# Optimization experiments

Measured on AMD Instinct MI355X. Metric: run time of the kernel, lower is better.

## Reference

```python
import jax, jax.numpy as jnp
import numpy as np

NUM_Q_HEADS = 64
NUM_KV_HEADS = 8
HEAD_DIM = 64
HIDDEN = 2880
SLIDING_WINDOW = 128
ROPE_WAVELENGTH = 10000.0
NEG_INF = jnp.float32(-1e9)


def _rope(x, start_index=0):
    # x: (b, s, n, h). yarn with scaling_factor=1.0 == standard RoPE (split-half rotate).
    s, h = x.shape[1], x.shape[-1]
    inv_freq = 1.0 / (ROPE_WAVELENGTH ** (jnp.arange(0, h, 2, dtype=jnp.float32) / h))
    pos = jnp.arange(s, dtype=jnp.float32) + start_index
    freqs = pos[:, None] * inv_freq[None, :]  # (s, h/2)
    cos = jnp.concatenate([jnp.cos(freqs), jnp.cos(freqs)], axis=-1)[None, :, None, :]
    sin = jnp.concatenate([jnp.sin(freqs), jnp.sin(freqs)], axis=-1)[None, :, None, :]
    x1, x2 = jnp.split(x, 2, axis=-1)
    rot = jnp.concatenate([-x2, x1], axis=-1)
    return x * cos + rot * sin


def setup_inputs() -> dict:
    key = jax.random.key(0)
    ks = jax.random.split(key, 9)
    b, s = 1, 2048
    scale = 0.02
    hidden_states = jax.random.normal(ks[0], (b, s, HIDDEN), jnp.float32)
    Wq = jax.random.normal(ks[1], (HIDDEN, NUM_Q_HEADS, HEAD_DIM), jnp.float32) * scale
    Wk = jax.random.normal(ks[2], (HIDDEN, NUM_KV_HEADS, HEAD_DIM), jnp.float32) * scale
    Wv = jax.random.normal(ks[3], (HIDDEN, NUM_KV_HEADS, HEAD_DIM), jnp.float32) * scale
    Wo = jax.random.normal(ks[4], (NUM_Q_HEADS, HEAD_DIM, HIDDEN), jnp.float32) * scale
    bq = jnp.zeros((NUM_Q_HEADS, HEAD_DIM), jnp.float32)
    bk = jnp.zeros((NUM_KV_HEADS, HEAD_DIM), jnp.float32)
    bv = jnp.zeros((NUM_KV_HEADS, HEAD_DIM), jnp.float32)
    bo = jnp.zeros((HIDDEN,), jnp.float32)
    sinks = jax.random.normal(ks[5], (NUM_Q_HEADS,), jnp.float32) * 0.05
    attention_mask = jnp.tril(jnp.ones((s, s), bool))[None]  # causal, (b, q, k)
    return dict(hidden_states=hidden_states, Wq=Wq, bq=bq, Wk=Wk, bk=bk, Wv=Wv,
                bv=bv, Wo=Wo, bo=bo, sinks=sinks, attention_mask=attention_mask)


def reference(hidden_states, Wq, bq, Wk, bk, Wv, bv, Wo, bo, sinks, attention_mask):
    b, s, _ = hidden_states.shape
    inv_norm = 1.0 / np.sqrt(HEAD_DIM).astype(np.float32)
    # QKV projections (EinsumDense with bias)
    q = jnp.einsum('bqm,muh->bquh', hidden_states, Wq) + bq
    k = jnp.einsum('bkm,mvh->bkvh', hidden_states, Wk) + bk
    v = jnp.einsum('bkm,mvh->bkvh', hidden_states, Wv) + bv
    # rotary_dim == head_dim (even), so RoPE applies to the full head dim
    q = _rope(q)
    k = _rope(k)
    # GQA: repeat kv heads
    groups = NUM_Q_HEADS // NUM_KV_HEADS
    k = jnp.repeat(k, groups, axis=2)
    v = jnp.repeat(v, groups, axis=2)
    scores = jnp.einsum('bquh,bkuh->buqk', q, k) * inv_norm
    # sliding-window mask: keep kv_pos >= q_pos - window
    qpos = jnp.arange(s)
    swin = qpos[None, :] >= qpos[:, None] - SLIDING_WINDOW  # (q, k)
    scores = jnp.where(swin[None, None], scores, NEG_INF)
    scores = jnp.where(attention_mask[:, None], scores, NEG_INF)
    # sink-token logit per head appended as extra kv column
    sink = jnp.broadcast_to(sinks.reshape(1, NUM_Q_HEADS, 1, 1), (b, NUM_Q_HEADS, s, 1))
    logits = jnp.concatenate([scores, sink], axis=-1)
    m = jax.lax.stop_gradient(jnp.max(logits, axis=-1, keepdims=True))
    probs = jax.nn.softmax(logits - m, axis=-1)[..., :-1]  # drop sink column
    attn = jnp.einsum('buqk,bkuh->bquh', probs, v)
    return jnp.einsum('bquh,uhm->bqm', attn, Wo) + bo
```

## Files before the change

kernel.cpp:

```cpp
#include <hip/hip_runtime.h>
#include <cstdint>

typedef __attribute__((ext_vector_type(4))) float f32x4;
typedef __attribute__((ext_vector_type(8))) short bf16x8;

#define HIDDEN 2880
#define SEQ 2048
#define QKV_N 5120
#define WIN 128

__device__ __forceinline__ ushort f2bf(float f) {
  uint32_t u = __builtin_bit_cast(uint32_t, f);
  u += 0x7fff + ((u >> 16) & 1);
  return (ushort)(u >> 16);
}
__device__ __forceinline__ float bf2f(ushort h) {
  uint32_t u = ((uint32_t)h) << 16;
  return __builtin_bit_cast(float, u);
}

__global__ void conv_kernel(const float* __restrict__ in, ushort* __restrict__ out, int n) {
  int i = (blockIdx.x * blockDim.x + threadIdx.x) * 8;
  if (i >= n) return;
  float4 a = *(const float4*)(in + i);
  float4 b = *(const float4*)(in + i + 4);
  bf16x8 o;
  o[0] = (short)f2bf(a.x); o[1] = (short)f2bf(a.y); o[2] = (short)f2bf(a.z); o[3] = (short)f2bf(a.w);
  o[4] = (short)f2bf(b.x); o[5] = (short)f2bf(b.y); o[6] = (short)f2bf(b.z); o[7] = (short)f2bf(b.w);
  *(bf16x8*)(out + i) = o;
}

__global__ __launch_bounds__(256) void tconv2_kernel(const float* __restrict__ in, ushort* __restrict__ out,
                                                     int C, int out_ld, int out_row_off) {
  __shared__ ushort tile[64][68];
  int c0 = blockIdx.x * 64, r0 = blockIdx.y * 64;
  int t = threadIdx.x;
  int lr = t >> 4;
  int lc = (t & 15) * 4;
#pragma unroll
  for (int i = 0; i < 4; ++i) {
    float4 v = *(const float4*)&in[(size_t)(r0 + i * 16 + lr) * C + c0 + lc];
    ushort4 o;
    o.x = f2bf(v.x); o.y = f2bf(v.y); o.z = f2bf(v.z); o.w = f2bf(v.w);
    *(ushort4*)&tile[i * 16 + lr][lc] = o;
  }
  __syncthreads();
  int rr0 = (t & 7) * 8;
#pragma unroll
  for (int i2 = 0; i2 < 2; ++i2) {
    int cc = i2 * 32 + (t >> 3);
    bf16x8 o;
#pragma unroll
    for (int j = 0; j < 8; ++j) o[j] = (short)tile[rr0 + j][cc];
    *(bf16x8*)&out[(size_t)(out_row_off + c0 + cc) * out_ld + r0 + rr0] = o;
  }
}

__global__ void biascat_kernel(const float* __restrict__ bq, const float* __restrict__ bk,
                               const float* __restrict__ bv, float* __restrict__ out) {
  int i = blockIdx.x * blockDim.x + threadIdx.x;
  if (i >= QKV_N) return;
  float v = (i < 4096) ? bq[i] : (i < 4608) ? bk[i - 4096] : bv[i - 4608];
  out[i] = v;
}

__global__ void ropetab_kernel(float2* __restrict__ tab) {
  int i = blockIdx.x * blockDim.x + threadIdx.x;
  int s = i >> 5, d = i & 31;
  float inv = powf(10000.0f, -(float)d / 32.0f);
  float f = (float)s * inv;
  tab[i] = make_float2(cosf(f), sinf(f));
}

__global__ void rope8_kernel(ushort* __restrict__ buf, const float2* __restrict__ tab,
                             int perrow , int total) {
  int idx = blockIdx.x * blockDim.x + threadIdx.x;
  if (idx >= total) return;
  int s = idx / perrow;
  int p = idx - s * perrow;
  int head = p >> 2, j = p & 3;
  ushort* base = buf + (size_t)s * QKV_N + head * 64 + j * 8;
  bf16x8 x1 = *(const bf16x8*)base;
  bf16x8 x2 = *(const bf16x8*)(base + 32);
  bf16x8 o1, o2;
#pragma unroll
  for (int i = 0; i < 8; ++i) {
    float2 cs = tab[(s << 5) + j * 8 + i];
    float a = bf2f((ushort)x1[i]), b = bf2f((ushort)x2[i]);
    o1[i] = (short)f2bf(a * cs.x - b * cs.y);
    o2[i] = (short)f2bf(b * cs.x + a * cs.y);
  }
  *(bf16x8*)base = o1;
  *(bf16x8*)(base + 32) = o2;
}

__global__ __launch_bounds__(256) void vt_kernel(const ushort* __restrict__ qkv, ushort* __restrict__ vt) {
  __shared__ ushort tile[64][80];
  int kv0 = blockIdx.x * 64, d0 = blockIdx.y * 64;
  int t = threadIdx.x;
#pragma unroll
  for (int p = 0; p < 2; ++p) {
    int lr = p * 32 + (t >> 3);
    *(bf16x8*)&tile[lr][(t & 7) * 8] =
        *(const bf16x8*)&qkv[(size_t)(kv0 + lr) * QKV_N + 4608 + d0 + (t & 7) * 8];
  }
  __syncthreads();
#pragma unroll
  for (int p = 0; p < 2; ++p) {
    int dl = p * 32 + (t >> 3);
    bf16x8 o;
#pragma unroll
    for (int jj = 0; jj < 8; ++jj) o[jj] = (short)tile[(t & 7) * 8 + jj][dl];
    *(bf16x8*)&vt[(size_t)(d0 + dl) * 2048 + kv0 + (t & 7) * 8] = o;
  }
}

template <int BN, bool OUT_BF16>
__global__ __launch_bounds__(256, 2) void gemm4w_kernel(
    const ushort* __restrict__ A, const ushort* __restrict__ Bt,
    const float* __restrict__ bias, void* __restrict__ Cv,
    int K, int lda, int ldb, int ldc) {
  constexpr int NFRAG = BN / 32;
  constexpr int BHALF = BN * 64;
  constexpr int BCHUNKS = BHALF / 1024;
  constexpr int BUFBYTES = 16384 + 2 * BHALF;
  __shared__ __align__(16) char ldsbuf[2 * BUFBYTES];

  const int cpx = gridDim.x >> 3;
  const int wg = ((int)blockIdx.x & 7) * cpx + ((int)blockIdx.x >> 3);
  const int mtile = wg & 15, ntile = wg >> 4;
  const int m0 = mtile * 128, n0 = ntile * BN;

  const int tid = threadIdx.x, wv = tid >> 6, l = tid & 63;
  const int wm = wv >> 1, wn = wv & 1;
  const int r = l & 15, g = l >> 4;

  const int c = l ^ ((l >> 3) & 3);
  const ushort* gA0 = A + (size_t)(m0 + (c >> 2)) * lda + (c & 3) * 8;
  const ushort* gB0 = Bt + (size_t)(n0 + (c >> 2)) * ldb + (c & 3) * 8;

  const int gsw = (g * 16) ^ (((r >> 1) & 3) << 4);
  const int aOff = (wm * 64 + r) * 64 + gsw;
  const int bOff = (wn * (NFRAG * 16) + r) * 64 + gsw;

  auto sA = [&](int nb, int kg, int kh) {
#pragma unroll
    for (int j = 0; j < 2; ++j) {
      int cid = j * 4 + wv;
      __builtin_amdgcn_global_load_lds(
          (const __attribute__((address_space(1))) void*)(const void*)(gA0 + (size_t)cid * 16 * lda + kg),
          (__attribute__((address_space(3))) void*)&ldsbuf[nb * BUFBYTES + kh * 8192 + cid * 1024], 16, 0, 0);
    }
  };
  auto sB = [&](int nb, int kg, int kh) {
#pragma unroll
    for (int j = 0; j < (BCHUNKS + 3) / 4; ++j) {
      int cid = j * 4 + wv;
      if (cid < BCHUNKS)
        __builtin_amdgcn_global_load_lds(
            (const __attribute__((address_space(1))) void*)(const void*)(gB0 + (size_t)cid * 16 * ldb + kg),
            (__attribute__((address_space(3))) void*)&ldsbuf[nb * BUFBYTES + 16384 + kh * BHALF + cid * 1024],
            16, 0, 0);
    }
  };

#define BAR() __builtin_amdgcn_s_barrier()
#define LGKM0()                                              \
  do {                                                       \
    asm volatile("s_waitcnt lgkmcnt(0)" ::: "memory");       \
    __builtin_amdgcn_sched_barrier(0);                       \
  } while (0)
#define WAITV0() asm volatile("s_waitcnt vmcnt(0)" ::: "memory")

  f32x4 acc[4][NFRAG] = {};
  const int nt = K >> 6;

  sA(0, 0, 0); sA(0, 32, 1); sB(0, 0, 0); sB(0, 32, 1);
  WAITV0();
  BAR();

  for (int t = 0; t < nt; ++t) {
    const int bufOff = (t & 1) * BUFBYTES;
    const int nb = (t & 1) ^ 1;
    if (t + 1 < nt) {
      const int kn = (t + 1) * 64;
      sA(nb, kn, 0); sA(nb, kn + 32, 1);
      sB(nb, kn, 0); sB(nb, kn + 32, 1);
    }
#pragma unroll
    for (int kh = 0; kh < 2; ++kh) {
      bf16x8 aq[4], bq[NFRAG];
#pragma unroll
      for (int nf = 0; nf < NFRAG; ++nf)
        bq[nf] = *(const bf16x8*)&ldsbuf[bufOff + 16384 + kh * BHALF + bOff + nf * 1024];
#pragma unroll
      for (int mi = 0; mi < 4; ++mi)
        aq[mi] = *(const bf16x8*)&ldsbuf[bufOff + kh * 8192 + aOff + mi * 1024];
      LGKM0();
      __builtin_amdgcn_s_setprio(1);
#pragma unroll
      for (int mi = 0; mi < 4; ++mi)
#pragma unroll
        for (int nf = 0; nf < NFRAG; ++nf)
          acc[mi][nf] = __builtin_amdgcn_mfma_f32_16x16x32_bf16(aq[mi], bq[nf], acc[mi][nf], 0, 0, 0);
      __builtin_amdgcn_s_setprio(0);
    }
    WAITV0();
    BAR();
  }

#pragma unroll
  for (int mf2 = 0; mf2 < 4; ++mf2) {
#pragma unroll
    for (int nf = 0; nf < NFRAG; ++nf) {
      int cc = n0 + wn * (NFRAG * 16) + nf * 16 + r;
      float b = bias[cc];
#pragma unroll
      for (int j = 0; j < 4; ++j) {
        int rrow = m0 + wm * 64 + mf2 * 16 + g * 4 + j;
        float v = acc[mf2][nf][j] + b;
        if (OUT_BF16) ((ushort*)Cv)[(size_t)rrow * ldc + cc] = f2bf(v);
        else ((float*)Cv)[(size_t)rrow * ldc + cc] = v;
      }
    }
  }
#undef BAR
#undef LGKM0
#undef WAITV0
}

__global__ __launch_bounds__(512, 4) void attn_kernel(
    const ushort* __restrict__ qkv, const ushort* __restrict__ vt,
    const float* __restrict__ sinks, ushort* __restrict__ out) {
  __shared__ __align__(16) char lds[54272];
  const int kh = blockIdx.y;
  const int q0 = blockIdx.x * 32;
  const int kvw0 = q0 - 128;
  const int tid = threadIdx.x, w = tid >> 6, l = tid & 63;
  const int r = l & 15, g = l >> 4;
  const int h = kh * 8 + w;

  if (tid < 256) ((uint32_t*)(lds + 40960))[tid] = 0;

#pragma unroll
  for (int it = 0; it < 3; ++it) {
    int c = it * 512 + tid;
    if (c < 1280) {
      {
        int row = c >> 3, ch = c & 7;
        int kv = kvw0 + row;
        bf16x8 vv = {};
        if (kv >= 0) vv = *(const bf16x8*)&qkv[(size_t)kv * QKV_N + 4096 + kh * 64 + ch * 8];
        int byte = (row * 128 + ch * 16) ^ ((row & 7) << 4);
        *(bf16x8*)(lds + byte) = vv;
      }
      {
        int row = c / 20, ch = c - (c / 20) * 20;
        int kv = kvw0 + ch * 8;
        bf16x8 vv = {};
        if (kv >= 0) vv = *(const bf16x8*)&vt[(size_t)(kh * 64 + row) * 2048 + kv];
        int byte = (row * 320 + ch * 16) ^ ((row & 7) << 4);
        *(bf16x8*)(lds + 20480 + byte) = vv;
      }
    }
  }
  __syncthreads();

  char* Pw = lds + 41984 + w * 1536;
  const float snk = sinks[h];

#pragma unroll
  for (int si = 0; si < 2; ++si) {
    const ushort* qb = &qkv[(size_t)(q0 + si * 16 + r) * QKV_N + h * 64 + g * 8];
    bf16x8 qf0 = *(const bf16x8*)qb;
    bf16x8 qf1 = *(const bf16x8*)(qb + 32);

    f32x4 S[9];
    float mx[4] = {-3e30f, -3e30f, -3e30f, -3e30f};
#pragma unroll
    for (int tt = 0; tt < 9; ++tt) {
      int kvloc = (si + tt) * 16 + r;
      int b0 = (kvloc * 128 + g * 16) ^ ((kvloc & 7) << 4);
      int b1 = (kvloc * 128 + 64 + g * 16) ^ ((kvloc & 7) << 4);
      bf16x8 kf0 = *(const bf16x8*)(lds + b0);
      bf16x8 kf1 = *(const bf16x8*)(lds + b1);
      f32x4 s = {};
      s = __builtin_amdgcn_mfma_f32_16x16x32_bf16(qf0, kf0, s, 0, 0, 0);
      s = __builtin_amdgcn_mfma_f32_16x16x32_bf16(qf1, kf1, s, 0, 0, 0);
      int kvc = kvw0 + kvloc;
#pragma unroll
      for (int j = 0; j < 4; ++j) {
        int qr = q0 + si * 16 + g * 4 + j;
        bool valid = (kvc >= 0) && (kvc <= qr) && (kvc >= qr - WIN);
        float v = valid ? s[j] * 0.125f : -1e30f;
        s[j] = v;
        mx[j] = fmaxf(mx[j], v);
      }
      S[tt] = s;
    }
#pragma unroll
    for (int off = 1; off < 16; off <<= 1)
#pragma unroll
      for (int j = 0; j < 4; ++j) mx[j] = fmaxf(mx[j], __shfl_xor(mx[j], off, 64));
    float m[4], sum[4] = {0, 0, 0, 0};
#pragma unroll
    for (int j = 0; j < 4; ++j) m[j] = fmaxf(mx[j], snk);
#pragma unroll
    for (int tt = 0; tt < 9; ++tt)
#pragma unroll
      for (int j = 0; j < 4; ++j) {
        float p = (S[tt][j] > -1e29f) ? __expf(S[tt][j] - m[j]) : 0.0f;
        S[tt][j] = p;
        sum[j] += p;
      }
#pragma unroll
    for (int off = 1; off < 16; off <<= 1)
#pragma unroll
      for (int j = 0; j < 4; ++j) sum[j] += __shfl_xor(sum[j], off, 64);
    float rinv[4];
#pragma unroll
    for (int j = 0; j < 4; ++j) rinv[j] = 1.0f / (sum[j] + __expf(snk - m[j]));

    f32x4 acc[4] = {};
#pragma unroll
    for (int ks = 0; ks < 5; ++ks) {
#pragma unroll
      for (int c2 = 0; c2 < 2; ++c2) {
        int tt = 2 * ks + c2;
#pragma unroll
        for (int j = 0; j < 4; ++j) {
          float pv = (tt <= 8) ? S[tt][j] * rinv[j] : 0.0f;
          *(ushort*)(Pw + ((g * 4 + j) * 48 + c2 * 16 + r) * 2) = f2bf(pv);
        }
      }
      bf16x8 pa = *(const bf16x8*)(Pw + (r * 48 + g * 8) * 2);
#pragma unroll
      for (int ni = 0; ni < 4; ++ni) {
        int row = ni * 16 + r;
        int byte = (row * 320 + (si * 16 + ks * 32 + g * 8) * 2) ^ ((row & 7) << 4);
        bf16x8 vb = *(const bf16x8*)(lds + 20480 + byte);
        acc[ni] = __builtin_amdgcn_mfma_f32_16x16x32_bf16(pa, vb, acc[ni], 0, 0, 0);
      }
    }
#pragma unroll
    for (int ni = 0; ni < 4; ++ni)
#pragma unroll
      for (int j = 0; j < 4; ++j)
        out[(size_t)(q0 + si * 16 + g * 4 + j) * 4096 + h * 64 + ni * 16 + r] = f2bf(acc[ni][j]);
  }
}

extern "C" void kernel_launch(void* const* d_in, const int* in_sizes, int n_in,
                              void* d_out, int out_size, void* d_ws, size_t ws_size,
                              hipStream_t stream) {
  const float* hs = (const float*)d_in[0];
  const float* Wq = (const float*)d_in[1];
  const float* bq = (const float*)d_in[2];
  const float* Wk = (const float*)d_in[3];
  const float* bk = (const float*)d_in[4];
  const float* Wv = (const float*)d_in[5];
  const float* bv = (const float*)d_in[6];
  const float* Wo = (const float*)d_in[7];
  const float* bo = (const float*)d_in[8];
  const float* sinks = (const float*)d_in[9];
  float* out = (float*)d_out;

  char* ws = (char*)d_ws;
  ushort* hs_bf   = (ushort*)(ws + 0);
  ushort* vt_g    = (ushort*)(ws + 0);
  ushort* wqkv_t  = (ushort*)(ws + 11796480);
  ushort* attn    = (ushort*)(ws + 11796480);
  ushort* wo_t    = (ushort*)(ws + 41287680);
  ushort* qkv     = (ushort*)(ws + 66453504);
  float*  bias_all= (float*)(ws + 87425024);
  float2* tab     = (float2*)(ws + 87445504);

  conv_kernel<<<5898240 / 8 / 256, 256, 0, stream>>>(hs, hs_bf, 5898240);
  tconv2_kernel<<<dim3(64, 45), 256, 0, stream>>>(Wq, wqkv_t, 4096, 2880, 0);
  tconv2_kernel<<<dim3(8, 45), 256, 0, stream>>>(Wk, wqkv_t, 512, 2880, 4096);
  tconv2_kernel<<<dim3(8, 45), 256, 0, stream>>>(Wv, wqkv_t, 512, 2880, 4608);
  tconv2_kernel<<<dim3(45, 64), 256, 0, stream>>>(Wo, wo_t, 2880, 4096, 0);
  biascat_kernel<<<20, 256, 0, stream>>>(bq, bk, bv, bias_all);
  ropetab_kernel<<<2048 * 32 / 256, 256, 0, stream>>>(tab);

  gemm4w_kernel<160, true><<<512, 256, 0, stream>>>(hs_bf, wqkv_t, bias_all, qkv,
                                                    2880, 2880, 2880, 5120);
  rope8_kernel<<<2048, 256, 0, stream>>>(qkv, tab, 256, 2048 * 256);
  rope8_kernel<<<256, 256, 0, stream>>>(qkv + 4096, tab, 32, 2048 * 32);
  vt_kernel<<<dim3(32, 8), 256, 0, stream>>>(qkv, vt_g);
  attn_kernel<<<dim3(64, 8), 512, 0, stream>>>(qkv, vt_g, sinks, attn);
  gemm4w_kernel<160, false><<<288, 256, 0, stream>>>(attn, wo_t, bo, out,
                                                     4096, 4096, 4096, 2880);
}
```

Before: 208.6 us.

## Fuse RoPE into attention, prefetch both LDS halves in GEMM, widen output tile

Removes the two standalone RoPE kernels and applies the rotation inside the attention kernel, to K while staging it into LDS and to Q fragments after loading. This saves a full read-modify-write pass over Q and K in global memory and two launches. The cost is that K rows are re-rotated redundantly in every block whose window overlaps them. Separately, the GEMM main loop issues both k-halves' LDS fragment loads up front and waits with a partial lgkmcnt, so the second half's loads overlap the first half's MFMAs. The output projection GEMM also switches its N tile from 160 to 192 with fewer blocks.

Result: faster. 202.7 us (-2.8%).

```diff
diff --git a/kernel.cpp b/kernel.cpp
--- a/kernel.cpp
+++ b/kernel.cpp
@@ -70,28 +70,6 @@
   float inv = powf(10000.0f, -(float)d / 32.0f);
   float f = (float)s * inv;
   tab[i] = make_float2(cosf(f), sinf(f));
-}
-
-__global__ void rope8_kernel(ushort* __restrict__ buf, const float2* __restrict__ tab,
-                             int perrow , int total) {
-  int idx = blockIdx.x * blockDim.x + threadIdx.x;
-  if (idx >= total) return;
-  int s = idx / perrow;
-  int p = idx - s * perrow;
-  int head = p >> 2, j = p & 3;
-  ushort* base = buf + (size_t)s * QKV_N + head * 64 + j * 8;
-  bf16x8 x1 = *(const bf16x8*)base;
-  bf16x8 x2 = *(const bf16x8*)(base + 32);
-  bf16x8 o1, o2;
-#pragma unroll
-  for (int i = 0; i < 8; ++i) {
-    float2 cs = tab[(s << 5) + j * 8 + i];
-    float a = bf2f((ushort)x1[i]), b = bf2f((ushort)x2[i]);
-    o1[i] = (short)f2bf(a * cs.x - b * cs.y);
-    o2[i] = (short)f2bf(b * cs.x + a * cs.y);
-  }
-  *(bf16x8*)base = o1;
-  *(bf16x8*)(base + 32) = o2;
 }
 
 __global__ __launch_bounds__(256) void vt_kernel(const ushort* __restrict__ qkv, ushort* __restrict__ vt) {
@@ -165,10 +143,10 @@
   };
 
 #define BAR() __builtin_amdgcn_s_barrier()
-#define LGKM0()                                              \
-  do {                                                       \
-    asm volatile("s_waitcnt lgkmcnt(0)" ::: "memory");       \
-    __builtin_amdgcn_sched_barrier(0);                       \
+#define LGKMC(N)                                                       \
+  do {                                                                 \
+    asm volatile("s_waitcnt lgkmcnt(%0)" ::"n"(N) : "memory");         \
+    __builtin_amdgcn_sched_barrier(0);                                 \
   } while (0)
 #define WAITV0() asm volatile("s_waitcnt vmcnt(0)" ::: "memory")
 
@@ -182,29 +160,41 @@
   for (int t = 0; t < nt; ++t) {
     const int bufOff = (t & 1) * BUFBYTES;
     const int nb = (t & 1) ^ 1;
+    bf16x8 aq0[4], bq0[NFRAG], aq1[4], bq1[NFRAG];
+#pragma unroll
+    for (int nf = 0; nf < NFRAG; ++nf)
+      bq0[nf] = *(const bf16x8*)&ldsbuf[bufOff + 16384 + bOff + nf * 1024];
+#pragma unroll
+    for (int mi = 0; mi < 4; ++mi)
+      aq0[mi] = *(const bf16x8*)&ldsbuf[bufOff + aOff + mi * 1024];
+    __builtin_amdgcn_sched_barrier(0);
+#pragma unroll
+    for (int nf = 0; nf < NFRAG; ++nf)
+      bq1[nf] = *(const bf16x8*)&ldsbuf[bufOff + 16384 + BHALF + bOff + nf * 1024];
+#pragma unroll
+    for (int mi = 0; mi < 4; ++mi)
+      aq1[mi] = *(const bf16x8*)&ldsbuf[bufOff + 8192 + aOff + mi * 1024];
     if (t + 1 < nt) {
       const int kn = (t + 1) * 64;
       sA(nb, kn, 0); sA(nb, kn + 32, 1);
       sB(nb, kn, 0); sB(nb, kn + 32, 1);
     }
-#pragma unroll
-    for (int kh = 0; kh < 2; ++kh) {
-      bf16x8 aq[4], bq[NFRAG];
+    LGKMC(4 + NFRAG);
+    __builtin_amdgcn_s_setprio(1);
+#pragma unroll
+    for (int mi = 0; mi < 4; ++mi)
 #pragma unroll
       for (int nf = 0; nf < NFRAG; ++nf)
-        bq[nf] = *(const bf16x8*)&ldsbuf[bufOff + 16384 + kh * BHALF + bOff + nf * 1024];
-#pragma unroll
-      for (int mi = 0; mi < 4; ++mi)
-        aq[mi] = *(const bf16x8*)&ldsbuf[bufOff + kh * 8192 + aOff + mi * 1024];
-      LGKM0();
-      __builtin_amdgcn_s_setprio(1);
-#pragma unroll
-      for (int mi = 0; mi < 4; ++mi)
-#pragma unroll
-        for (int nf = 0; nf < NFRAG; ++nf)
-          acc[mi][nf] = __builtin_amdgcn_mfma_f32_16x16x32_bf16(aq[mi], bq[nf], acc[mi][nf], 0, 0, 0);
-      __builtin_amdgcn_s_setprio(0);
-    }
+        acc[mi][nf] = __builtin_amdgcn_mfma_f32_16x16x32_bf16(aq0[mi], bq0[nf], acc[mi][nf], 0, 0, 0);
+    __builtin_amdgcn_s_setprio(0);
+    LGKMC(0);
+    __builtin_amdgcn_s_setprio(1);
+#pragma unroll
+    for (int mi = 0; mi < 4; ++mi)
+#pragma unroll
+      for (int nf = 0; nf < NFRAG; ++nf)
+        acc[mi][nf] = __builtin_amdgcn_mfma_f32_16x16x32_bf16(aq1[mi], bq1[nf], acc[mi][nf], 0, 0, 0);
+    __builtin_amdgcn_s_setprio(0);
     WAITV0();
     BAR();
   }
@@ -225,13 +215,14 @@
     }
   }
 #undef BAR
-#undef LGKM0
+#undef LGKMC
 #undef WAITV0
 }
 
 __global__ __launch_bounds__(512, 4) void attn_kernel(
     const ushort* __restrict__ qkv, const ushort* __restrict__ vt,
-    const float* __restrict__ sinks, ushort* __restrict__ out) {
+    const float* __restrict__ sinks, const float2* __restrict__ tab,
+    ushort* __restrict__ out) {
   __shared__ __align__(16) char lds[54272];
   const int kh = blockIdx.y;
   const int q0 = blockIdx.x * 32;
@@ -243,25 +234,36 @@
   if (tid < 256) ((uint32_t*)(lds + 40960))[tid] = 0;
 
 #pragma unroll
-  for (int it = 0; it < 3; ++it) {
+  for (int it = 0; it < 4; ++it) {
     int c = it * 512 + tid;
-    if (c < 1280) {
-      {
-        int row = c >> 3, ch = c & 7;
-        int kv = kvw0 + row;
-        bf16x8 vv = {};
-        if (kv >= 0) vv = *(const bf16x8*)&qkv[(size_t)kv * QKV_N + 4096 + kh * 64 + ch * 8];
-        int byte = (row * 128 + ch * 16) ^ ((row & 7) << 4);
-        *(bf16x8*)(lds + byte) = vv;
-      }
-      {
-        int row = c / 20, ch = c - (c / 20) * 20;
-        int kv = kvw0 + ch * 8;
-        bf16x8 vv = {};
-        if (kv >= 0) vv = *(const bf16x8*)&vt[(size_t)(kh * 64 + row) * 2048 + kv];
-        int byte = (row * 320 + ch * 16) ^ ((row & 7) << 4);
-        *(bf16x8*)(lds + 20480 + byte) = vv;
-      }
+    if (c < 640) {
+      int row = c >> 2, ch = c & 3;
+      int kv = kvw0 + row;
+      bf16x8 v1 = {}, v2 = {};
+      if (kv >= 0) {
+        const ushort* kb = &qkv[(size_t)kv * QKV_N + 4096 + kh * 64 + ch * 8];
+        bf16x8 x1 = *(const bf16x8*)kb;
+        bf16x8 x2 = *(const bf16x8*)(kb + 32);
+#pragma unroll
+        for (int i = 0; i < 8; ++i) {
+          float2 cs = tab[(kv << 5) + ch * 8 + i];
+          float a = bf2f((ushort)x1[i]), b = bf2f((ushort)x2[i]);
+          v1[i] = (short)f2bf(a * cs.x - b * cs.y);
+          v2[i] = (short)f2bf(b * cs.x + a * cs.y);
+        }
+      }
+      int b1 = (row * 128 + ch * 16) ^ ((row & 7) << 4);
+      int b2 = (row * 128 + (ch + 4) * 16) ^ ((row & 7) << 4);
+      *(bf16x8*)(lds + b1) = v1;
+      *(bf16x8*)(lds + b2) = v2;
+    } else if (c < 1920) {
+      int cv = c - 640;
+      int row = cv / 20, ch = cv - (cv / 20) * 20;
+      int kv = kvw0 + ch * 8;
+      bf16x8 vv = {};
+      if (kv >= 0) vv = *(const bf16x8*)&vt[(size_t)(kh * 64 + row) * 2048 + kv];
+      int byte = (row * 320 + ch * 16) ^ ((row & 7) << 4);
+      *(bf16x8*)(lds + 20480 + byte) = vv;
     }
   }
   __syncthreads();
@@ -274,6 +276,18 @@
     const ushort* qb = &qkv[(size_t)(q0 + si * 16 + r) * QKV_N + h * 64 + g * 8];
     bf16x8 qf0 = *(const bf16x8*)qb;
     bf16x8 qf1 = *(const bf16x8*)(qb + 32);
+    {
+      int s = q0 + si * 16 + r;
+      bf16x8 t0, t1;
+#pragma unroll
+      for (int i = 0; i < 8; ++i) {
+        float2 cs = tab[(s << 5) + g * 8 + i];
+        float a = bf2f((ushort)qf0[i]), b = bf2f((ushort)qf1[i]);
+        t0[i] = (short)f2bf(a * cs.x - b * cs.y);
+        t1[i] = (short)f2bf(b * cs.x + a * cs.y);
+      }
+      qf0 = t0; qf1 = t1;
+    }
 
     f32x4 S[9];
     float mx[4] = {-3e30f, -3e30f, -3e30f, -3e30f};
@@ -385,10 +399,8 @@
 
   gemm4w_kernel<160, true><<<512, 256, 0, stream>>>(hs_bf, wqkv_t, bias_all, qkv,
                                                     2880, 2880, 2880, 5120);
-  rope8_kernel<<<2048, 256, 0, stream>>>(qkv, tab, 256, 2048 * 256);
-  rope8_kernel<<<256, 256, 0, stream>>>(qkv + 4096, tab, 32, 2048 * 32);
   vt_kernel<<<dim3(32, 8), 256, 0, stream>>>(qkv, vt_g);
-  attn_kernel<<<dim3(64, 8), 512, 0, stream>>>(qkv, vt_g, sinks, attn);
-  gemm4w_kernel<160, false><<<288, 256, 0, stream>>>(attn, wo_t, bo, out,
+  attn_kernel<<<dim3(64, 8), 512, 0, stream>>>(qkv, vt_g, sinks, tab, attn);
+  gemm4w_kernel<192, false><<<240, 256, 0, stream>>>(attn, wo_t, bo, out,
                                                      4096, 4096, 4096, 2880);
 }
```
